# Performance work log

Hardware: AMD Instinct MI355X
Metric: run time of the kernel (lower is better)

Reference implementation:

```python
import jax, jax.numpy as jnp
import numpy as np

STRIDES = (2, 2, 2, 2)
ALPHA = 1.0
NEG_SLOPE = 0.1


def _conv1d(h, w, b, stride):
    # h: (N, C, L), w: (O, I, K) -> (N, O, L_out), VALID padding
    out = jax.lax.conv_general_dilated(
        h, w, window_strides=(stride,), padding='VALID',
        dimension_numbers=('NCH', 'OIH', 'NCH'))
    return out + b[None, :, None]


def setup_inputs() -> dict:
    key = jax.random.key(0)
    ks = jax.random.split(key, 10)
    N, C, L = 256, 128, 1024
    k_sizes = (15, 12, 7, 4)
    inp = {'x': jax.random.normal(ks[0], (N, C, L), dtype=jnp.float32)}
    for i, k in enumerate(k_sizes):
        fan_in = C * k
        scale = 1.0 / np.sqrt(fan_in).astype(np.float32)
        inp[f'w{i+1}'] = jax.random.normal(ks[1 + 2 * i], (C, C, k), dtype=jnp.float32) * scale
        inp[f'b{i+1}'] = jax.random.normal(ks[2 + 2 * i], (C,), dtype=jnp.float32) * 0.01
    D = C * 59  # flattened encoder output: 1024->505->247->121->59
    inp['centers'] = jax.random.normal(ks[9], (64, D), dtype=jnp.float32)
    return inp


def reference(x, w1, b1, w2, b2, w3, b3, w4, b4, centers):
    ws = [(w1, b1), (w2, b2), (w3, b3), (w4, b4)]
    h = x
    for i, ((w, b), s) in enumerate(zip(ws, STRIDES)):
        h = _conv1d(h, w, b, s)
        if i != len(ws) - 1:
            h = jnp.where(h > 0, h, NEG_SLOPE * h)  # LeakyReLU(0.1)
    z = h.reshape(h.shape[0], -1)  # (N, D)
    # squared distances via norm expansion: ||z||^2 + ||c||^2 - 2 z.c
    d2 = (jnp.sum(z * z, axis=1, keepdims=True)
          + jnp.sum(centers * centers, axis=1)[None, :]
          - 2.0 * z @ centers.T)  # (N, K)
    q = 1.0 / (1.0 + d2 / ALPHA)
    q = q ** ((ALPHA + 1.0) / 2.0)
    q = q / jnp.sum(q, axis=1, keepdims=True)
    return q
```

## Files before the change

kernel.cpp:

```cpp
#include <hip/hip_runtime.h>

typedef __bf16 bf16;
typedef __bf16 bf16x4 __attribute__((ext_vector_type(4)));
typedef __bf16 bf16x8 __attribute__((ext_vector_type(8)));
typedef float f32x4 __attribute__((ext_vector_type(4)));

#define CCH 128

__global__ void k_prep_all(const float* __restrict__ w1, const float* __restrict__ w2,
                           const float* __restrict__ w3, const float* __restrict__ w4,
                           const float* __restrict__ cen,
                           bf16* __restrict__ o1, bf16* __restrict__ o2,
                           bf16* __restrict__ o3, bf16* __restrict__ o4,
                           bf16* __restrict__ cpk, float* __restrict__ cc) {
    __shared__ float red[256];
    int tid = threadIdx.x;
    int bid = blockIdx.x;
    if (bid < 2432) {
        int idx = bid * 256 + tid;
        const float* src; bf16* dst; int Kw; int r = idx;
        if (r < 15 * 16384) { src = w1; dst = o1; Kw = 15; }
        else if ((r -= 15 * 16384) < 12 * 16384) { src = w2; dst = o2; Kw = 12; }
        else if ((r -= 12 * 16384) < 7 * 16384) { src = w3; dst = o3; Kw = 7; }
        else if ((r -= 7 * 16384) < 4 * 16384) { src = w4; dst = o4; Kw = 4; }
        else return;
        int e = r & 7, lane = (r >> 3) & 63, og = (r >> 9) & 7, c = (r >> 12) & 3, kt = r >> 14;
        int o = og * 16 + (lane & 15);
        int i = c * 32 + (lane >> 4) * 8 + e;
        dst[r] = (bf16)src[(o * 128 + i) * Kw + kt];
    } else if (bid < 2432 + 256) {
        int j = bid - 2432;
        int l = j >> 2;
#pragma unroll
        for (int it = 0; it < 8; ++it) {
            int u = tid + it * 256;
            int og = u >> 9, r9 = u & 511;
            int lane = r9 >> 3, e = r9 & 7;
            int k = og * 16 + (lane & 15);
            int oc = (j & 3) * 32 + (lane >> 4) * 8 + e;
            float v = (l < 59) ? cen[k * 7552 + oc * 59 + l] : 0.f;
            cpk[(((size_t)(j * 4 + og)) << 9) + r9] = (bf16)v;
        }
    } else {
        int k = bid - (2432 + 256);
        float s = 0.f;
        for (int idx = tid; idx < 8192; idx += 256) {
            int l = idx >> 7;
            int o = idx & 127;
            if (l < 59) {
                float fv = (float)(bf16)cen[k * 7552 + o * 59 + l];
                s += fv * fv;
            }
        }
        red[tid] = s;
        __syncthreads();
        for (int st = 128; st > 0; st >>= 1) {
            if (tid < st) red[tid] += red[tid + st];
            __syncthreads();
        }
        if (tid == 0) cc[k] = red[0];
    }
}

__global__ __launch_bounds__(256, 4) void k_conv1(
    const float* __restrict__ x, const bf16* __restrict__ wTp,
    const float* __restrict__ bias, bf16* __restrict__ out) {
    constexpr int KW = 15, LT = 128, PH = 2, OUT_ROWS = 512;
    constexpr int P = (LT - 1) * 2 + KW;
    constexpr int KC = 2;
    constexpr int RS = 64;
    constexpr int NLT = LT / 16;
    constexpr int ESE = 136;
    constexpr int SMELE = (P * RS > LT * ESE) ? P * RS : LT * ESE;
    constexpr int NJ = KW * KC;
    __shared__ __align__(16) bf16 smem[SMELE];

    const int n = blockIdx.y;
    const int l0 = blockIdx.x * LT;
    const int p0 = l0 * 2;
    const int tid = threadIdx.x;
    const int wid = tid >> 6;
    const int lane = tid & 63;
    const int quad = lane >> 4;
    const int l15 = lane & 15;
    const int og0 = wid * 2;

    f32x4 acc[2][NLT];
#pragma unroll
    for (int a = 0; a < 2; ++a)
#pragma unroll
        for (int b = 0; b < NLT; ++b) acc[a][b] = (f32x4){0.f, 0.f, 0.f, 0.f};

    bf16x8 afr[2][2];
    const bf16* wbase = wTp + (size_t)lane * 8;
    afr[0][0] = *(const bf16x8*)(wbase + ((size_t)(og0 + 0) << 9));
    afr[0][1] = *(const bf16x8*)(wbase + ((size_t)(og0 + 1) << 9));

    const int cst = tid >> 2;
    const int qw = tid & 3;

#pragma unroll 1
    for (int ph = 0; ph < PH; ++ph) {
        if (ph) __syncthreads();

        const float* bch = x + ((size_t)(n * 128 + ph * 64 + cst)) * 1024;
#pragma unroll 4
        for (int it = 0; it < 17; ++it) {
            int pp = it * 16 + qw * 4;
            int gp = p0 + pp;
            f32x4 t;
            if (gp + 3 < 1024) {
                t = *(const f32x4*)(bch + gp);
            } else {
#pragma unroll
                for (int e = 0; e < 4; ++e) t[e] = (gp + e < 1024) ? bch[gp + e] : 0.f;
            }
#pragma unroll
            for (int e = 0; e < 4; ++e) {
                int ppe = pp + e;
                int sc8 = (((cst >> 3) ^ ((ppe >> 1) & 7)) << 3) | (cst & 7);
                smem[ppe * RS + sc8] = (bf16)t[e];
            }
        }
        __syncthreads();

#pragma unroll 2
        for (int j = 0; j < NJ; ++j) {
            int nj = j + 1, nph = ph;
            if (nj == NJ) { nj = 0; ++nph; }
            if (nph < PH) {
                int kt1 = nj >> 1;
                int c1 = (nj & (KC - 1)) + nph * KC;
                const bf16* wp = wbase + ((size_t)((kt1 * 4 + c1) * 8 + og0) << 9);
                afr[(j + 1) & 1][0] = *(const bf16x8*)(wp);
                afr[(j + 1) & 1][1] = *(const bf16x8*)(wp + 512);
            }
            const int kt = j >> 1;
            const int c16l = (j & (KC - 1)) * 4 + quad;
#pragma unroll
            for (int lt = 0; lt < NLT; ++lt) {
                int p = (lt * 16 + l15) * 2 + kt;
                int sc = c16l ^ ((p >> 1) & 7);
                bf16x8 bfr = *(const bf16x8*)(smem + p * RS + sc * 8);
                acc[0][lt] = __builtin_amdgcn_mfma_f32_16x16x32_bf16(
                    afr[j & 1][0], bfr, acc[0][lt], 0, 0, 0);
                acc[1][lt] = __builtin_amdgcn_mfma_f32_16x16x32_bf16(
                    afr[j & 1][1], bfr, acc[1][lt], 0, 0, 0);
            }
        }
    }

    __syncthreads();
#pragma unroll
    for (int ot = 0; ot < 2; ++ot) {
        const int o0 = wid * 32 + ot * 16 + quad * 4;
        const f32x4 bv = *(const f32x4*)(bias + o0);
#pragma unroll
        for (int lt = 0; lt < NLT; ++lt) {
            const int l = lt * 16 + l15;
            bf16x4 pk;
#pragma unroll
            for (int r = 0; r < 4; ++r) {
                float v = acc[ot][lt][r] + bv[r];
                v = (v > 0.f) ? v : 0.1f * v;
                pk[r] = (bf16)v;
            }
            *(bf16x4*)(smem + l * ESE + o0) = pk;
        }
    }
    __syncthreads();
    constexpr int SNIT = LT * 16 / 256;
    bf16* op = out + ((size_t)n * OUT_ROWS + l0) * CCH;
#pragma unroll
    for (int it = 0; it < SNIT; ++it) {
        int u = tid + it * 256;
        int l = u >> 4;
        int g = u & 15;
        *(bf16x8*)(op + l * CCH + g * 8) = *(const bf16x8*)(smem + l * ESE + g * 8);
    }
}

__global__ __launch_bounds__(512, 1) void k_fused234(
    const bf16* __restrict__ h1g, const bf16* __restrict__ wT2,
    const bf16* __restrict__ wT3, const bf16* __restrict__ wT4,
    const float* __restrict__ b2, const float* __restrict__ b3,
    const float* __restrict__ b4, const bf16* __restrict__ cpk,
    const float* __restrict__ cc, float* __restrict__ out) {
    __shared__ __align__(16) bf16 lds[34048 + 33536];
    __shared__ float d2p[2][64];
    __shared__ float zred[8];
    bf16* sbuf = lds;
    bf16* h2   = lds + 34048;
    bf16* h3   = lds;
    bf16* zmem = lds + 16640;

    const int n = blockIdx.x;
    const int tid = threadIdx.x;
    const int wid = tid >> 6;
    const int lane = tid & 63;
    const int quad = lane >> 4;
    const int l15 = lane & 15;
    const int oh = wid & 1;
    const int rg = wid >> 1;

    if (tid < 96) *(f32x4*)(h2 + 256 * 128 + tid * 8) = (f32x4){0.f, 0.f, 0.f, 0.f};

    {
        const bf16* w2base = wT2 + (size_t)lane * 8 + ((size_t)(oh * 4) << 9);
        const bf16* base = h1g + (size_t)n * 512 * 128;
        constexpr int NJ2 = 48;
#pragma unroll 1
        for (int s = 0; s < 2; ++s) {
            if (s) __syncthreads();
#pragma unroll
            for (int it = 0; it < 9; ++it) {
                int u = tid + it * 512;
                if (u < 266 * 16) {
                    int p = u >> 4, c = u & 15;
                    int prow = s * 256 + p; if (prow > 511) prow = 511;
                    bf16x8 t = *(const bf16x8*)(base + (size_t)prow * 128 + c * 8);
                    int sc = (c & 8) | ((c & 7) ^ ((p >> 1) & 7));
                    *(bf16x8*)(sbuf + p * 128 + sc * 8) = t;
                }
            }
            __syncthreads();

            f32x4 acc[4][2];
#pragma unroll
            for (int a = 0; a < 4; ++a)
#pragma unroll
                for (int b = 0; b < 2; ++b) acc[a][b] = (f32x4){0.f, 0.f, 0.f, 0.f};
            bf16x8 afr[2][4];
#pragma unroll
            for (int a = 0; a < 4; ++a)
                afr[0][a] = *(const bf16x8*)(w2base + ((size_t)a << 9));
#pragma unroll 2
            for (int j = 0; j < NJ2; ++j) {
                if (j + 1 < NJ2) {
                    int kt1 = (j + 1) >> 2, c1 = (j + 1) & 3;
                    const bf16* wp = w2base + ((size_t)((kt1 * 4 + c1) * 8) << 9);
#pragma unroll
                    for (int a = 0; a < 4; ++a)
                        afr[(j + 1) & 1][a] = *(const bf16x8*)(wp + ((size_t)a << 9));
                }
                int kt = j >> 2;
                int c16l = (j & 3) * 4 + quad;
#pragma unroll
                for (int lt = 0; lt < 2; ++lt) {
                    int p = (rg * 32 + lt * 16 + l15) * 2 + kt;
                    int sc = (c16l & 8) | ((c16l & 7) ^ ((p >> 1) & 7));
                    bf16x8 bfr = *(const bf16x8*)(sbuf + p * 128 + sc * 8);
#pragma unroll
                    for (int a = 0; a < 4; ++a)
                        acc[a][lt] = __builtin_amdgcn_mfma_f32_16x16x32_bf16(
                            afr[j & 1][a], bfr, acc[a][lt], 0, 0, 0);
                }
            }
#pragma unroll
            for (int a = 0; a < 4; ++a) {
                int o0 = (oh * 4 + a) * 16 + quad * 4;
                f32x4 bv = *(const f32x4*)(b2 + o0);
                int c = o0 >> 3;
#pragma unroll
                for (int lt = 0; lt < 2; ++lt) {
                    int l = s * 128 + rg * 32 + lt * 16 + l15;
                    bf16x4 pk;
#pragma unroll
                    for (int r = 0; r < 4; ++r) {
                        float v = acc[a][lt][r] + bv[r];
                        v = (v > 0.f) ? v : 0.1f * v;
                        pk[r] = (bf16)v;
                    }
                    int sc = (c & 8) | ((c & 7) ^ ((l >> 1) & 7));
                    *(bf16x4*)(h2 + l * 128 + sc * 8 + (o0 & 7)) = pk;
                }
            }
        }
        __syncthreads();
    }

    {
        if (tid < 32) *(f32x4*)(h3 + 128 * 128 + tid * 8) = (f32x4){0.f, 0.f, 0.f, 0.f};
        const bf16* w3base = wT3 + (size_t)lane * 8 + ((size_t)(oh * 4) << 9);
        constexpr int NJ3 = 28;
        f32x4 acc[4][2];
#pragma unroll
        for (int a = 0; a < 4; ++a)
#pragma unroll
            for (int b = 0; b < 2; ++b) acc[a][b] = (f32x4){0.f, 0.f, 0.f, 0.f};
        bf16x8 afr[2][4];
#pragma unroll
        for (int a = 0; a < 4; ++a)
            afr[0][a] = *(const bf16x8*)(w3base + ((size_t)a << 9));
#pragma unroll 2
        for (int j = 0; j < NJ3; ++j) {
            if (j + 1 < NJ3) {
                int kt1 = (j + 1) >> 2, c1 = (j + 1) & 3;
                const bf16* wp = w3base + ((size_t)((kt1 * 4 + c1) * 8) << 9);
#pragma unroll
                for (int a = 0; a < 4; ++a)
                    afr[(j + 1) & 1][a] = *(const bf16x8*)(wp + ((size_t)a << 9));
            }
            int kt = j >> 2;
            int c16l = (j & 3) * 4 + quad;
#pragma unroll
            for (int lt = 0; lt < 2; ++lt) {
                int p = (rg * 32 + lt * 16 + l15) * 2 + kt;
                int sc = (c16l & 8) | ((c16l & 7) ^ ((p >> 1) & 7));
                bf16x8 bfr = *(const bf16x8*)(h2 + p * 128 + sc * 8);
#pragma unroll
                for (int a = 0; a < 4; ++a)
                    acc[a][lt] = __builtin_amdgcn_mfma_f32_16x16x32_bf16(
                        afr[j & 1][a], bfr, acc[a][lt], 0, 0, 0);
            }
        }
        __syncthreads();
#pragma unroll
        for (int a = 0; a < 4; ++a) {
            int o0 = (oh * 4 + a) * 16 + quad * 4;
            f32x4 bv = *(const f32x4*)(b3 + o0);
            int c = o0 >> 3;
#pragma unroll
            for (int lt = 0; lt < 2; ++lt) {
                int l = rg * 32 + lt * 16 + l15;
                bf16x4 pk;
#pragma unroll
                for (int r = 0; r < 4; ++r) {
                    float v = acc[a][lt][r] + bv[r];
                    v = (v > 0.f) ? v : 0.1f * v;
                    pk[r] = (bf16)v;
                }
                int sc = (c & 8) | ((c & 7) ^ ((l >> 1) & 7));
                *(bf16x4*)(h3 + l * 128 + sc * 8 + (o0 & 7)) = pk;
            }
        }
    }
    __syncthreads();

    {
        f32x4 acc[4];
#pragma unroll
        for (int a = 0; a < 4; ++a) acc[a] = (f32x4){0.f, 0.f, 0.f, 0.f};
        bf16x8 afr[2][4];
        const bf16* w4base = wT4 + (size_t)lane * 8 + ((size_t)(oh * 4) << 9);
#pragma unroll
        for (int a = 0; a < 4; ++a)
            afr[0][a] = *(const bf16x8*)(w4base + ((size_t)a << 9));
        constexpr int NJ4 = 16;
#pragma unroll 2
        for (int j = 0; j < NJ4; ++j) {
            if (j + 1 < NJ4) {
                int kt1 = (j + 1) >> 2, c1 = (j + 1) & 3;
                const bf16* wp = w4base + ((size_t)((kt1 * 4 + c1) * 8) << 9);
#pragma unroll
                for (int a = 0; a < 4; ++a)
                    afr[(j + 1) & 1][a] = *(const bf16x8*)(wp + ((size_t)a << 9));
            }
            int kt = j >> 2;
            int c16l = (j & 3) * 4 + quad;
            int p = (rg * 16 + l15) * 2 + kt;
            int sc = (c16l & 8) | ((c16l & 7) ^ ((p >> 1) & 7));
            bf16x8 bfr = *(const bf16x8*)(h3 + p * 128 + sc * 8);
#pragma unroll
            for (int a = 0; a < 4; ++a)
                acc[a] = __builtin_amdgcn_mfma_f32_16x16x32_bf16(
                    afr[j & 1][a], bfr, acc[a], 0, 0, 0);
        }
        const int l = rg * 16 + l15;
        float s2 = 0.f;
#pragma unroll
        for (int a = 0; a < 4; ++a) {
            const int o0 = (oh * 4 + a) * 16 + quad * 4;
            const f32x4 bv = *(const f32x4*)(b4 + o0);
            bf16x4 pk;
#pragma unroll
            for (int r = 0; r < 4; ++r) {
                float v = acc[a][r] + bv[r];
                pk[r] = (l < 59) ? (bf16)v : (bf16)0.f;
                float zf = (float)pk[r];
                s2 += zf * zf;
            }
            *(bf16x4*)(zmem + l * 136 + o0) = pk;
        }
#pragma unroll
        for (int o = 32; o > 0; o >>= 1) s2 += __shfl_xor(s2, o);
        if (lane == 0) zred[wid] = s2;
    }
    __syncthreads();

    {
        const int og = wid & 3;
        const int h = wid >> 2;
        const bf16* cb = cpk + ((size_t)og << 9) + (size_t)lane * 8;
        f32x4 acc = (f32x4){0.f, 0.f, 0.f, 0.f};
        const int j0 = h * 128;
        bf16x8 af[4];
#pragma unroll
        for (int q = 0; q < 4; ++q)
            af[q] = *(const bf16x8*)(cb + ((size_t)(j0 + q) << 11));
#pragma unroll 4
        for (int jj = 0; jj < 128; ++jj) {
            bf16x8 a = af[jj & 3];
            if (jj + 4 < 128)
                af[jj & 3] = *(const bf16x8*)(cb + ((size_t)(j0 + jj + 4) << 11));
            int l = h * 32 + (jj >> 2);
            int off = (jj & 3) * 32 + quad * 8;
            bf16x8 b = *(const bf16x8*)(zmem + l * 136 + off);
            acc = __builtin_amdgcn_mfma_f32_16x16x32_bf16(a, b, acc, 0, 0, 0);
        }
        if (l15 == 0) {
#pragma unroll
            for (int r = 0; r < 4; ++r) d2p[h][og * 16 + quad * 4 + r] = acc[r];
        }
    }
    __syncthreads();

    if (tid < 64) {
        float zc = d2p[0][tid] + d2p[1][tid];
        float z2 = zred[0] + zred[1] + zred[2] + zred[3]
                 + zred[4] + zred[5] + zred[6] + zred[7];
        float d2v = z2 + cc[tid] - 2.f * zc;
        float q = 1.f / (1.f + d2v);
        float tot = q;
#pragma unroll
        for (int o = 32; o > 0; o >>= 1) tot += __shfl_xor(tot, o);
        out[n * 64 + tid] = q / tot;
    }
}

extern "C" void kernel_launch(void* const* d_in, const int* in_sizes, int n_in,
                              void* d_out, int out_size, void* d_ws, size_t ws_size,
                              hipStream_t stream) {
    (void)in_sizes; (void)n_in; (void)out_size; (void)ws_size;
    const float* x   = (const float*)d_in[0];
    const float* w1  = (const float*)d_in[1];
    const float* b1  = (const float*)d_in[2];
    const float* w2  = (const float*)d_in[3];
    const float* b2  = (const float*)d_in[4];
    const float* w3  = (const float*)d_in[5];
    const float* b3  = (const float*)d_in[6];
    const float* w4  = (const float*)d_in[7];
    const float* b4  = (const float*)d_in[8];
    const float* cen = (const float*)d_in[9];
    float* out = (float*)d_out;

    char* ws = (char*)d_ws;
    size_t off = 0;
    auto alloc = [&](size_t bytes) -> void* {
        void* p = ws + off;
        off += (bytes + 255) & ~(size_t)255;
        return p;
    };
    bf16* wT1 = (bf16*)alloc((size_t)15 * 16384 * sizeof(bf16));
    bf16* wT2 = (bf16*)alloc((size_t)12 * 16384 * sizeof(bf16));
    bf16* wT3 = (bf16*)alloc((size_t)7 * 16384 * sizeof(bf16));
    bf16* wT4 = (bf16*)alloc((size_t)4 * 16384 * sizeof(bf16));
    bf16* cpk = (bf16*)alloc((size_t)1024 * 512 * sizeof(bf16));
    float* cc = (float*)alloc(64 * sizeof(float));
    bf16* h1  = (bf16*)alloc((size_t)256 * 512 * 128 * sizeof(bf16));
    (void)alloc((size_t)1 << 20);

    k_prep_all<<<2432 + 256 + 64, 256, 0, stream>>>(w1, w2, w3, w4, cen,
                                                    wT1, wT2, wT3, wT4, cpk, cc);
    k_conv1<<<dim3(4, 256), 256, 0, stream>>>(x, wT1, b1, h1);
    k_fused234<<<256, 512, 0, stream>>>(h1, wT2, wT3, wT4, b2, b3, b4, cpk, cc, out);
}
```

Before: 321.0 us.

## Double fused conv2-4 block to 1024 threads with finer per-wave work split

Raises the fused conv2/3/4 + soft-assignment kernel from 512 to 1024 threads per block. Each wave now handles 16 output positions instead of 32 in conv2/conv3, half the output channels in conv4, and a quarter of the K range in the distance GEMM, with the partial-reduction buffers enlarged to match. The intent is more waves per CU to hide latency, since the grid has only 256 blocks with one block per CU. In exchange, weight-fragment loads are reused across fewer MFMAs, and the register budget per thread is tighter.

```diff
diff --git a/kernel.cpp b/kernel.cpp
--- a/kernel.cpp
+++ b/kernel.cpp
@@ -180,15 +180,15 @@
     }
 }
 
-__global__ __launch_bounds__(512, 1) void k_fused234(
+__global__ __launch_bounds__(1024, 1) void k_fused234(
     const bf16* __restrict__ h1g, const bf16* __restrict__ wT2,
     const bf16* __restrict__ wT3, const bf16* __restrict__ wT4,
     const float* __restrict__ b2, const float* __restrict__ b3,
     const float* __restrict__ b4, const bf16* __restrict__ cpk,
     const float* __restrict__ cc, float* __restrict__ out) {
     __shared__ __align__(16) bf16 lds[34048 + 33536];
-    __shared__ float d2p[2][64];
-    __shared__ float zred[8];
+    __shared__ float d2p[4][64];
+    __shared__ float zred[16];
     bf16* sbuf = lds;
     bf16* h2   = lds + 34048;
     bf16* h3   = lds;
@@ -200,12 +200,12 @@
     const int lane = tid & 63;
     const int quad = lane >> 4;
     const int l15 = lane & 15;
-    const int oh = wid & 1;
-    const int rg = wid >> 1;
 
     if (tid < 96) *(f32x4*)(h2 + 256 * 128 + tid * 8) = (f32x4){0.f, 0.f, 0.f, 0.f};
 
     {
+        const int oh = wid & 1;
+        const int rg = wid >> 1;
         const bf16* w2base = wT2 + (size_t)lane * 8 + ((size_t)(oh * 4) << 9);
         const bf16* base = h1g + (size_t)n * 512 * 128;
         constexpr int NJ2 = 48;
@@ -213,8 +213,8 @@
         for (int s = 0; s < 2; ++s) {
             if (s) __syncthreads();
 #pragma unroll
-            for (int it = 0; it < 9; ++it) {
-                int u = tid + it * 512;
+            for (int it = 0; it < 5; ++it) {
+                int u = tid + it * 1024;
                 if (u < 266 * 16) {
                     int p = u >> 4, c = u & 15;
                     int prow = s * 256 + p; if (prow > 511) prow = 511;
@@ -225,11 +225,9 @@
             }
             __syncthreads();
 
-            f32x4 acc[4][2];
-#pragma unroll
-            for (int a = 0; a < 4; ++a)
-#pragma unroll
-                for (int b = 0; b < 2; ++b) acc[a][b] = (f32x4){0.f, 0.f, 0.f, 0.f};
+            f32x4 acc[4];
+#pragma unroll
+            for (int a = 0; a < 4; ++a) acc[a] = (f32x4){0.f, 0.f, 0.f, 0.f};
             bf16x8 afr[2][4];
 #pragma unroll
             for (int a = 0; a < 4; ++a)
@@ -245,35 +243,29 @@
                 }
                 int kt = j >> 2;
                 int c16l = (j & 3) * 4 + quad;
-#pragma unroll
-                for (int lt = 0; lt < 2; ++lt) {
-                    int p = (rg * 32 + lt * 16 + l15) * 2 + kt;
-                    int sc = (c16l & 8) | ((c16l & 7) ^ ((p >> 1) & 7));
-                    bf16x8 bfr = *(const bf16x8*)(sbuf + p * 128 + sc * 8);
-#pragma unroll
-                    for (int a = 0; a < 4; ++a)
-                        acc[a][lt] = __builtin_amdgcn_mfma_f32_16x16x32_bf16(
-                            afr[j & 1][a], bfr, acc[a][lt], 0, 0, 0);
-                }
-            }
+                int p = (rg * 16 + l15) * 2 + kt;
+                int sc = (c16l & 8) | ((c16l & 7) ^ ((p >> 1) & 7));
+                bf16x8 bfr = *(const bf16x8*)(sbuf + p * 128 + sc * 8);
+#pragma unroll
+                for (int a = 0; a < 4; ++a)
+                    acc[a] = __builtin_amdgcn_mfma_f32_16x16x32_bf16(
+                        afr[j & 1][a], bfr, acc[a], 0, 0, 0);
+            }
+            int l = s * 128 + rg * 16 + l15;
 #pragma unroll
             for (int a = 0; a < 4; ++a) {
                 int o0 = (oh * 4 + a) * 16 + quad * 4;
                 f32x4 bv = *(const f32x4*)(b2 + o0);
                 int c = o0 >> 3;
-#pragma unroll
-                for (int lt = 0; lt < 2; ++lt) {
-                    int l = s * 128 + rg * 32 + lt * 16 + l15;
-                    bf16x4 pk;
-#pragma unroll
-                    for (int r = 0; r < 4; ++r) {
-                        float v = acc[a][lt][r] + bv[r];
-                        v = (v > 0.f) ? v : 0.1f * v;
-                        pk[r] = (bf16)v;
-                    }
-                    int sc = (c & 8) | ((c & 7) ^ ((l >> 1) & 7));
-                    *(bf16x4*)(h2 + l * 128 + sc * 8 + (o0 & 7)) = pk;
+                bf16x4 pk;
+#pragma unroll
+                for (int r = 0; r < 4; ++r) {
+                    float v = acc[a][r] + bv[r];
+                    v = (v > 0.f) ? v : 0.1f * v;
+                    pk[r] = (bf16)v;
                 }
+                int sc = (c & 8) | ((c & 7) ^ ((l >> 1) & 7));
+                *(bf16x4*)(h2 + l * 128 + sc * 8 + (o0 & 7)) = pk;
             }
         }
         __syncthreads();
@@ -281,13 +273,13 @@
 
     {
         if (tid < 32) *(f32x4*)(h3 + 128 * 128 + tid * 8) = (f32x4){0.f, 0.f, 0.f, 0.f};
+        const int oh = wid & 1;
+        const int rg = wid >> 1;
         const bf16* w3base = wT3 + (size_t)lane * 8 + ((size_t)(oh * 4) << 9);
         constexpr int NJ3 = 28;
-        f32x4 acc[4][2];
-#pragma unroll
-        for (int a = 0; a < 4; ++a)
-#pragma unroll
-            for (int b = 0; b < 2; ++b) acc[a][b] = (f32x4){0.f, 0.f, 0.f, 0.f};
+        f32x4 acc[4];
+#pragma unroll
+        for (int a = 0; a < 4; ++a) acc[a] = (f32x4){0.f, 0.f, 0.f, 0.f};
         bf16x8 afr[2][4];
 #pragma unroll
         for (int a = 0; a < 4; ++a)
@@ -303,48 +295,44 @@
             }
             int kt = j >> 2;
             int c16l = (j & 3) * 4 + quad;
-#pragma unroll
-            for (int lt = 0; lt < 2; ++lt) {
-                int p = (rg * 32 + lt * 16 + l15) * 2 + kt;
-                int sc = (c16l & 8) | ((c16l & 7) ^ ((p >> 1) & 7));
-                bf16x8 bfr = *(const bf16x8*)(h2 + p * 128 + sc * 8);
-#pragma unroll
-                for (int a = 0; a < 4; ++a)
-                    acc[a][lt] = __builtin_amdgcn_mfma_f32_16x16x32_bf16(
-                        afr[j & 1][a], bfr, acc[a][lt], 0, 0, 0);
-            }
+            int p = (rg * 16 + l15) * 2 + kt;
+            int sc = (c16l & 8) | ((c16l & 7) ^ ((p >> 1) & 7));
+            bf16x8 bfr = *(const bf16x8*)(h2 + p * 128 + sc * 8);
+#pragma unroll
+            for (int a = 0; a < 4; ++a)
+                acc[a] = __builtin_amdgcn_mfma_f32_16x16x32_bf16(
+                    afr[j & 1][a], bfr, acc[a], 0, 0, 0);
         }
         __syncthreads();
+        int l = rg * 16 + l15;
 #pragma unroll
         for (int a = 0; a < 4; ++a) {
             int o0 = (oh * 4 + a) * 16 + quad * 4;
             f32x4 bv = *(const f32x4*)(b3 + o0);
             int c = o0 >> 3;
-#pragma unroll
-            for (int lt = 0; lt < 2; ++lt) {
-                int l = rg * 32 + lt * 16 + l15;
-                bf16x4 pk;
-#pragma unroll
-                for (int r = 0; r < 4; ++r) {
-                    float v = acc[a][lt][r] + bv[r];
-                    v = (v > 0.f) ? v : 0.1f * v;
-                    pk[r] = (bf16)v;
-                }
-                int sc = (c & 8) | ((c & 7) ^ ((l >> 1) & 7));
-                *(bf16x4*)(h3 + l * 128 + sc * 8 + (o0 & 7)) = pk;
-            }
+            bf16x4 pk;
+#pragma unroll
+            for (int r = 0; r < 4; ++r) {
+                float v = acc[a][r] + bv[r];
+                v = (v > 0.f) ? v : 0.1f * v;
+                pk[r] = (bf16)v;
+            }
+            int sc = (c & 8) | ((c & 7) ^ ((l >> 1) & 7));
+            *(bf16x4*)(h3 + l * 128 + sc * 8 + (o0 & 7)) = pk;
         }
     }
     __syncthreads();
 
     {
-        f32x4 acc[4];
-#pragma unroll
-        for (int a = 0; a < 4; ++a) acc[a] = (f32x4){0.f, 0.f, 0.f, 0.f};
-        bf16x8 afr[2][4];
-        const bf16* w4base = wT4 + (size_t)lane * 8 + ((size_t)(oh * 4) << 9);
-#pragma unroll
-        for (int a = 0; a < 4; ++a)
+        const int rg = wid & 3;
+        const int oq = wid >> 2;
+        f32x4 acc[2];
+#pragma unroll
+        for (int a = 0; a < 2; ++a) acc[a] = (f32x4){0.f, 0.f, 0.f, 0.f};
+        bf16x8 afr[2][2];
+        const bf16* w4base = wT4 + (size_t)lane * 8 + ((size_t)(oq * 2) << 9);
+#pragma unroll
+        for (int a = 0; a < 2; ++a)
             afr[0][a] = *(const bf16x8*)(w4base + ((size_t)a << 9));
         constexpr int NJ4 = 16;
 #pragma unroll 2
@@ -353,7 +341,7 @@
                 int kt1 = (j + 1) >> 2, c1 = (j + 1) & 3;
                 const bf16* wp = w4base + ((size_t)((kt1 * 4 + c1) * 8) << 9);
 #pragma unroll
-                for (int a = 0; a < 4; ++a)
+                for (int a = 0; a < 2; ++a)
                     afr[(j + 1) & 1][a] = *(const bf16x8*)(wp + ((size_t)a << 9));
             }
             int kt = j >> 2;
@@ -362,15 +350,15 @@
             int sc = (c16l & 8) | ((c16l & 7) ^ ((p >> 1) & 7));
             bf16x8 bfr = *(const bf16x8*)(h3 + p * 128 + sc * 8);
 #pragma unroll
-            for (int a = 0; a < 4; ++a)
+            for (int a = 0; a < 2; ++a)
                 acc[a] = __builtin_amdgcn_mfma_f32_16x16x32_bf16(
                     afr[j & 1][a], bfr, acc[a], 0, 0, 0);
         }
         const int l = rg * 16 + l15;
         float s2 = 0.f;
 #pragma unroll
-        for (int a = 0; a < 4; ++a) {
-            const int o0 = (oh * 4 + a) * 16 + quad * 4;
+        for (int a = 0; a < 2; ++a) {
+            const int o0 = (oq * 2 + a) * 16 + quad * 4;
             const f32x4 bv = *(const f32x4*)(b4 + o0);
             bf16x4 pk;
 #pragma unroll
@@ -390,35 +378,36 @@
 
     {
         const int og = wid & 3;
-        const int h = wid >> 2;
+        const int kq = wid >> 2;
         const bf16* cb = cpk + ((size_t)og << 9) + (size_t)lane * 8;
         f32x4 acc = (f32x4){0.f, 0.f, 0.f, 0.f};
-        const int j0 = h * 128;
+        const int j0 = kq * 64;
         bf16x8 af[4];
 #pragma unroll
         for (int q = 0; q < 4; ++q)
             af[q] = *(const bf16x8*)(cb + ((size_t)(j0 + q) << 11));
 #pragma unroll 4
-        for (int jj = 0; jj < 128; ++jj) {
+        for (int jj = 0; jj < 64; ++jj) {
             bf16x8 a = af[jj & 3];
-            if (jj + 4 < 128)
+            if (jj + 4 < 64)
                 af[jj & 3] = *(const bf16x8*)(cb + ((size_t)(j0 + jj + 4) << 11));
-            int l = h * 32 + (jj >> 2);
+            int l = kq * 16 + (jj >> 2);
             int off = (jj & 3) * 32 + quad * 8;
             bf16x8 b = *(const bf16x8*)(zmem + l * 136 + off);
             acc = __builtin_amdgcn_mfma_f32_16x16x32_bf16(a, b, acc, 0, 0, 0);
         }
         if (l15 == 0) {
 #pragma unroll
-            for (int r = 0; r < 4; ++r) d2p[h][og * 16 + quad * 4 + r] = acc[r];
+            for (int r = 0; r < 4; ++r) d2p[kq][og * 16 + quad * 4 + r] = acc[r];
         }
     }
     __syncthreads();
 
     if (tid < 64) {
-        float zc = d2p[0][tid] + d2p[1][tid];
-        float z2 = zred[0] + zred[1] + zred[2] + zred[3]
-                 + zred[4] + zred[5] + zred[6] + zred[7];
+        float zc = d2p[0][tid] + d2p[1][tid] + d2p[2][tid] + d2p[3][tid];
+        float z2 = 0.f;
+#pragma unroll
+        for (int w = 0; w < 16; ++w) z2 += zred[w];
         float d2v = z2 + cc[tid] - 2.f * zc;
         float q = 1.f / (1.f + d2v);
         float tot = q;
@@ -463,5 +452,5 @@
     k_prep_all<<<2432 + 256 + 64, 256, 0, stream>>>(w1, w2, w3, w4, cen,
                                                     wT1, wT2, wT3, wT4, cpk, cc);
     k_conv1<<<dim3(4, 256), 256, 0, stream>>>(x, wT1, b1, h1);
-    k_fused234<<<256, 512, 0, stream>>>(h1, wT2, wT3, wT4, b2, b3, b4, cpk, cc, out);
+    k_fused234<<<256, 1024, 0, stream>>>(h1, wT2, wT3, wT4, b2, b3, b4, cpk, cc, out);
 }
```

Result: slower. 342.8 us (+6.8%).
